# Kernel tuning notes

Measured on AMD Instinct MI355X. Metric: run time of the kernel, lower is better.

The kernel has to match this reference:

```python
import jax, jax.numpy as jnp
import numpy as np

NBINS = 256
EPS = 1e-7  # tf.keras.backend.epsilon()


def setup_inputs() -> dict:
    key = jax.random.key(0)
    x = jax.random.uniform(key, (32, 512, 512, 3), dtype=jnp.float32)
    return {"x": x}


def reference(x):
    # x: [B, H, W, 3] with values in [0, 1]
    B, H, W, C = x.shape
    bin_width = jnp.maximum(jnp.asarray(1.0 / NBINS, x.dtype), jnp.asarray(EPS, x.dtype))
    bins = jnp.floor(x / bin_width)
    bins = jnp.clip(bins, 0, NBINS - 1).astype(jnp.int32)  # [B, H, W, C]

    # [B, C, H*W] -> scatter-add histogram per (image, channel)
    flat = bins.transpose(0, 3, 1, 2).reshape(B * C, H * W)

    def hist_one(idx):
        return jnp.zeros((NBINS,), dtype=jnp.float32).at[idx].add(1.0)

    hists = jax.vmap(hist_one)(flat)  # [B*C, NBINS]
    hists = hists.reshape(B, C, NBINS)
    hists = hists / jnp.sum(hists, axis=-1, keepdims=True)
    return hists.transpose(0, 2, 1)  # [B, NBINS, C]
```

## Files before the change

kernel.cpp:

```cpp
#include <hip/hip_runtime.h>
#include <hip/hip_bf16.h>


#define NBINS      256
#define B_IMG      32
#define HW         (512 * 512)
#define CH         3
#define ELEM_IMG   (HW * CH)
#define F4_IMG     (ELEM_IMG / 4)
#define THREADS    256
#define BLK_IMG    64
#define THR_IMG    (THREADS * BLK_IMG)
#define F4_THR     (F4_IMG / THR_IMG)
#define OUT_ELEMS  (B_IMG * NBINS * CH)

typedef float floatx4 __attribute__((ext_vector_type(4)));

__global__ __launch_bounds__(THREADS) void zero_kernel(float* __restrict__ out) {
    int i = blockIdx.x * THREADS + threadIdx.x;
    if (i < OUT_ELEMS) out[i] = 0.0f;
}

__global__ __launch_bounds__(THREADS) void hist_kernel(const floatx4* __restrict__ x,
                                                       float* __restrict__ out) {
    __shared__ unsigned int hist[CH * NBINS];

    const int tid = threadIdx.x;
    for (int j = tid; j < CH * NBINS; j += THREADS) hist[j] = 0u;
    __syncthreads();

    const int b = blockIdx.y;
    const floatx4* __restrict__ xb = x + (size_t)b * F4_IMG;
    const int t = blockIdx.x * THREADS + tid;

#pragma unroll
    for (int i = 0; i < F4_THR; ++i) {
        const int f = t + i * THR_IMG;
        const floatx4 v = __builtin_nontemporal_load(&xb[f]);
        int c = (f * 4) % 3;

        int b0 = min(NBINS - 1, max(0, (int)(v.x * 256.0f)));
        atomicAdd(&hist[c * NBINS + b0], 1u);
        c = (c == 2) ? 0 : c + 1;

        int b1 = min(NBINS - 1, max(0, (int)(v.y * 256.0f)));
        atomicAdd(&hist[c * NBINS + b1], 1u);
        c = (c == 2) ? 0 : c + 1;

        int b2 = min(NBINS - 1, max(0, (int)(v.z * 256.0f)));
        atomicAdd(&hist[c * NBINS + b2], 1u);
        c = (c == 2) ? 0 : c + 1;

        int b3 = min(NBINS - 1, max(0, (int)(v.w * 256.0f)));
        atomicAdd(&hist[c * NBINS + b3], 1u);
    }

    __syncthreads();

    float* __restrict__ ob = out + (size_t)b * (NBINS * CH);
    for (int j = tid; j < CH * NBINS; j += THREADS) {
        unsigned int cnt = hist[j];
        if (cnt) {
            int c   = j >> 8;
            int bin = j & 255;
            atomicAdd(&ob[bin * CH + c], (float)cnt * (1.0f / (float)HW));
        }
    }
}

extern "C" void kernel_launch(void* const* d_in, const int* in_sizes, int n_in,
                              void* d_out, int out_size, void* d_ws, size_t ws_size,
                              hipStream_t stream) {
    const floatx4* x = (const floatx4*)d_in[0];
    float* out = (float*)d_out;

    zero_kernel<<<(OUT_ELEMS + THREADS - 1) / THREADS, THREADS, 0, stream>>>(out);

    dim3 grid(BLK_IMG, B_IMG);
    hist_kernel<<<grid, THREADS, 0, stream>>>(x, out);
}
```

Baseline: 148.3 us.

## Replace global float atomics with per-block partial histograms and a reduce kernel

Each histogram block now writes its shared-memory counts to a workspace partial buffer in output layout, and a separate reduce kernel sums the 64 partials per image and normalizes. This removes the zero kernel and contended global float atomics, at the cost of an extra kernel launch and roughly 6 MB of partial traffic. It also simplifies the channel index computation inside the hot loop. The old path is kept as a fallback when the workspace is too small.

After: 137.6 us. 7.2% less time.

```diff
diff --git a/kernel.cpp b/kernel.cpp
--- a/kernel.cpp
+++ b/kernel.cpp
@@ -1,5 +1,4 @@
 #include <hip/hip_runtime.h>
-#include <hip/hip_bf16.h>
 
 
 #define NBINS      256
@@ -12,7 +11,10 @@
 #define BLK_IMG    64
 #define THR_IMG    (THREADS * BLK_IMG)
 #define F4_THR     (F4_IMG / THR_IMG)
+#define PJ         (CH * NBINS)
+#define NPART      (B_IMG * BLK_IMG)
 #define OUT_ELEMS  (B_IMG * NBINS * CH)
+#define PART_BYTES ((size_t)NPART * PJ * sizeof(unsigned int))
 
 typedef float floatx4 __attribute__((ext_vector_type(4)));
 
@@ -21,51 +23,80 @@
     if (i < OUT_ELEMS) out[i] = 0.0f;
 }
 
+template <bool USE_PART>
 __global__ __launch_bounds__(THREADS) void hist_kernel(const floatx4* __restrict__ x,
+                                                       unsigned int* __restrict__ part,
                                                        float* __restrict__ out) {
-    __shared__ unsigned int hist[CH * NBINS];
+    __shared__ unsigned int hist[PJ];
 
     const int tid = threadIdx.x;
-    for (int j = tid; j < CH * NBINS; j += THREADS) hist[j] = 0u;
+    hist[tid] = 0u; hist[tid + 256] = 0u; hist[tid + 512] = 0u;
     __syncthreads();
 
     const int b = blockIdx.y;
     const floatx4* __restrict__ xb = x + (size_t)b * F4_IMG;
     const int t = blockIdx.x * THREADS + tid;
 
+    int c0 = t % 3;
+
 #pragma unroll
     for (int i = 0; i < F4_THR; ++i) {
-        const int f = t + i * THR_IMG;
-        const floatx4 v = __builtin_nontemporal_load(&xb[f]);
-        int c = (f * 4) % 3;
+        const floatx4 v = __builtin_nontemporal_load(&xb[t + i * THR_IMG]);
+        const int cB = (c0 == 2) ? 0 : c0 + 1;
+        const int cC = (cB == 2) ? 0 : cB + 1;
 
         int b0 = min(NBINS - 1, max(0, (int)(v.x * 256.0f)));
-        atomicAdd(&hist[c * NBINS + b0], 1u);
-        c = (c == 2) ? 0 : c + 1;
+        atomicAdd(&hist[(c0 << 8) + b0], 1u);
+        int b1 = min(NBINS - 1, max(0, (int)(v.y * 256.0f)));
+        atomicAdd(&hist[(cB << 8) + b1], 1u);
+        int b2 = min(NBINS - 1, max(0, (int)(v.z * 256.0f)));
+        atomicAdd(&hist[(cC << 8) + b2], 1u);
+        int b3 = min(NBINS - 1, max(0, (int)(v.w * 256.0f)));
+        atomicAdd(&hist[(c0 << 8) + b3], 1u);
 
-        int b1 = min(NBINS - 1, max(0, (int)(v.y * 256.0f)));
-        atomicAdd(&hist[c * NBINS + b1], 1u);
-        c = (c == 2) ? 0 : c + 1;
-
-        int b2 = min(NBINS - 1, max(0, (int)(v.z * 256.0f)));
-        atomicAdd(&hist[c * NBINS + b2], 1u);
-        c = (c == 2) ? 0 : c + 1;
-
-        int b3 = min(NBINS - 1, max(0, (int)(v.w * 256.0f)));
-        atomicAdd(&hist[c * NBINS + b3], 1u);
+        c0 = cB;
     }
 
     __syncthreads();
 
-    float* __restrict__ ob = out + (size_t)b * (NBINS * CH);
-    for (int j = tid; j < CH * NBINS; j += THREADS) {
-        unsigned int cnt = hist[j];
-        if (cnt) {
-            int c   = j >> 8;
-            int bin = j & 255;
-            atomicAdd(&ob[bin * CH + c], (float)cnt * (1.0f / (float)HW));
+    if (USE_PART) {
+        unsigned int* __restrict__ pb =
+            part + (size_t)(b * BLK_IMG + blockIdx.x) * PJ;
+#pragma unroll
+        for (int s = 0; s < 3; ++s) {
+            const int jo  = tid + s * THREADS;
+            const int c   = jo % 3;
+            const int bin = jo / 3;
+            pb[jo] = hist[(c << 8) + bin];
+        }
+    } else {
+        float* __restrict__ ob = out + (size_t)b * PJ;
+        for (int j = tid; j < PJ; j += THREADS) {
+            unsigned int cnt = hist[j];
+            if (cnt) {
+                int c = j >> 8, bin = j & 255;
+                atomicAdd(&ob[bin * CH + c], (float)cnt * (1.0f / (float)HW));
+            }
         }
     }
+}
+
+__global__ __launch_bounds__(THREADS) void reduce_kernel(const unsigned int* __restrict__ part,
+                                                         float* __restrict__ out) {
+    const int t  = blockIdx.x * THREADS + threadIdx.x;
+    const int b  = t / PJ;
+    const int jo = t - b * PJ;
+    const unsigned int* __restrict__ pb = part + (size_t)b * BLK_IMG * PJ + jo;
+
+    unsigned int s0 = 0, s1 = 0, s2 = 0, s3 = 0;
+#pragma unroll 8
+    for (int k = 0; k < BLK_IMG; k += 4) {
+        s0 += pb[(size_t)(k + 0) * PJ];
+        s1 += pb[(size_t)(k + 1) * PJ];
+        s2 += pb[(size_t)(k + 2) * PJ];
+        s3 += pb[(size_t)(k + 3) * PJ];
+    }
+    out[t] = (float)(s0 + s1 + s2 + s3) * (1.0f / (float)HW);
 }
 
 extern "C" void kernel_launch(void* const* d_in, const int* in_sizes, int n_in,
@@ -74,8 +105,14 @@
     const floatx4* x = (const floatx4*)d_in[0];
     float* out = (float*)d_out;
 
-    zero_kernel<<<(OUT_ELEMS + THREADS - 1) / THREADS, THREADS, 0, stream>>>(out);
+    dim3 grid(BLK_IMG, B_IMG);
 
-    dim3 grid(BLK_IMG, B_IMG);
-    hist_kernel<<<grid, THREADS, 0, stream>>>(x, out);
+    if (ws_size >= PART_BYTES) {
+        unsigned int* part = (unsigned int*)d_ws;
+        hist_kernel<true><<<grid, THREADS, 0, stream>>>(x, part, out);
+        reduce_kernel<<<OUT_ELEMS / THREADS, THREADS, 0, stream>>>(part, out);
+    } else {
+        zero_kernel<<<(OUT_ELEMS + THREADS - 1) / THREADS, THREADS, 0, stream>>>(out);
+        hist_kernel<false><<<grid, THREADS, 0, stream>>>(x, nullptr, out);
+    }
 }
```
